# Kernel tuning notes

Measured on AMD Instinct MI355X. Metric: run time of the kernel, lower is better.

## Reference

```python
import jax, jax.numpy as jnp
import numpy as np

N_NODES = 50000
N_EDGES = 800000
F_IN = 128
HEADS = 4
C_OUT = 32
NEG_SLOPE = 0.2
BN_EPS = 1e-5


def _add_self_loops(edge_index, edge_attr, n):
    # PyG fill_value='mean': self-loop attr = mean of incoming edge attrs per node (0 if none)
    src, dst = edge_index[0], edge_index[1]
    deg = jax.ops.segment_sum(jnp.ones_like(edge_attr[:, 0]), dst, num_segments=n)
    loop_attr = jax.ops.segment_sum(edge_attr, dst, num_segments=n) / jnp.maximum(deg, 1.0)[:, None]
    loop = jnp.arange(n)
    src2 = jnp.concatenate([src, loop])
    dst2 = jnp.concatenate([dst, loop])
    attr2 = jnp.concatenate([edge_attr, loop_attr], axis=0)
    return src2, dst2, attr2


def _segment_softmax(logits, seg, n):
    m = jax.ops.segment_max(logits, seg, num_segments=n)
    m = jnp.where(jnp.isfinite(m), m, 0.0)
    ex = jnp.exp(logits - m[seg])
    s = jax.ops.segment_sum(ex, seg, num_segments=n)
    return ex / s[seg]


def _gatv2(x, src, dst, eattr, Wl, bl, Wr, br, We, att, bias, n):
    # x: [n, F]; returns [n, HEADS*C_OUT]
    xl = (x @ Wl + bl).reshape(n, HEADS, C_OUT)
    xr = (x @ Wr + br).reshape(n, HEADS, C_OUT)
    ea = (eattr @ We).reshape(-1, HEADS, C_OUT)
    xlj = xl[src]                                   # [E, H, C] gather
    msg = jax.nn.leaky_relu(xlj + xr[dst] + ea, NEG_SLOPE)
    logits = jnp.einsum('ehc,hc->eh', msg, att)     # [E, H]
    alpha = _segment_softmax(logits, dst, n)
    out = jax.ops.segment_sum(xlj * alpha[..., None], dst, num_segments=n)
    return out.reshape(n, HEADS * C_OUT) + bias


def _batchnorm(x, gamma, beta):
    mu = x.mean(axis=0)
    var = x.var(axis=0)
    return gamma * (x - mu) * jax.lax.rsqrt(var + BN_EPS) + beta


def setup_inputs() -> dict:
    key = jax.random.key(0)
    ks = jax.random.split(key, 20)
    HC = HEADS * C_OUT
    s = 0.05
    inp = {
        'emb': jax.random.normal(ks[0], (N_NODES, F_IN), dtype=jnp.float32),
        'edge_index': jax.random.randint(ks[1], (2, N_EDGES), 0, N_NODES, dtype=jnp.int64),
        'edge_weight': jax.random.uniform(ks[2], (N_EDGES, 1), dtype=jnp.float32),
        'Wl1': jax.random.normal(ks[3], (F_IN, HC)) * s,
        'bl1': jnp.zeros((HC,), jnp.float32),
        'Wr1': jax.random.normal(ks[4], (F_IN, HC)) * s,
        'br1': jnp.zeros((HC,), jnp.float32),
        'We1': jax.random.normal(ks[5], (1, HC)) * s,
        'att1': jax.random.normal(ks[6], (HEADS, C_OUT)) * s,
        'bias1': jnp.zeros((HC,), jnp.float32),
        'gamma1': jnp.ones((HC,), jnp.float32),
        'beta1': jnp.zeros((HC,), jnp.float32),
        'Wl2': jax.random.normal(ks[7], (HC, HC)) * s,
        'bl2': jnp.zeros((HC,), jnp.float32),
        'Wr2': jax.random.normal(ks[8], (HC, HC)) * s,
        'br2': jnp.zeros((HC,), jnp.float32),
        'We2': jax.random.normal(ks[9], (1, HC)) * s,
        'att2': jax.random.normal(ks[10], (HEADS, C_OUT)) * s,
        'bias2': jnp.zeros((HC,), jnp.float32),
    }
    return inp


def reference(emb, edge_index, edge_weight, Wl1, bl1, Wr1, br1, We1, att1, bias1,
              gamma1, beta1, Wl2, bl2, Wr2, br2, We2, att2, bias2):
    n = emb.shape[0]
    src, dst, eattr = _add_self_loops(edge_index, edge_weight, n)
    h1 = _gatv2(emb, src, dst, eattr, Wl1, bl1, Wr1, br1, We1, att1, bias1, n)
    h1 = jax.nn.elu(_batchnorm(h1, gamma1, beta1))
    h2 = _gatv2(h1, src, dst, eattr, Wl2, bl2, Wr2, br2, We2, att2, bias2, n)
    # fusion: mean over [input_emb, h1, h2] along stacked axis
    return (emb + h1 + h2) / 3.0
```

## Files before the change

kernel.cpp:

```cpp
#include <hip/hip_runtime.h>
#include <hip/hip_bf16.h>
#include <math.h>

#define N_NODES 50000
#define N_EDGES 800000
#define HC 128
#define SLOT 64

#define BM 128
#define NBX ((N_NODES + BM - 1) / BM)
#define NB_EDGE ((N_EDGES / 4 + 255) / 256)

typedef short bh8 __attribute__((ext_vector_type(8)));
typedef float f4 __attribute__((ext_vector_type(4)));
typedef float f2 __attribute__((ext_vector_type(2)));

__device__ __forceinline__ unsigned int pk2(float a, float b) {
  return (unsigned int)__bfloat16_as_ushort(__float2bfloat16(a)) |
         ((unsigned int)__bfloat16_as_ushort(__float2bfloat16(b)) << 16);
}

__global__ __launch_bounds__(256) void k_wprep(
    const float* __restrict__ Wl1, const float* __restrict__ Wr1,
    const float* __restrict__ Wl2, const float* __restrict__ Wr2,
    unsigned short* __restrict__ WtAll, int* __restrict__ cursor,
    float* __restrict__ chsum, float* __restrict__ chsq) {
  int gid = blockIdx.x * 256 + threadIdx.x;
  int m = gid >> 14;
  int idx = gid & 16383;
  const float* src = (m == 0) ? Wl1 : (m == 1) ? Wr1 : (m == 2) ? Wl2 : Wr2;
  int k = idx >> 7, n = idx & 127;
  WtAll[((size_t)m * HC + n) * HC + k] =
      __bfloat16_as_ushort(__float2bfloat16(src[k * HC + n]));
  if (gid < N_NODES) cursor[gid] = 0;
  if (gid < HC) { chsum[gid] = 0.f; chsq[gid] = 0.f; }
}

template <int LAYER2, int F8>
__device__ __forceinline__ void gemm_tile(
    int bx, const float* __restrict__ X, const unsigned short* __restrict__ Wt,
    const float* __restrict__ b0, const float* __restrict__ b1,
    void* __restrict__ Y0, float* __restrict__ Y1,
    const float* __restrict__ chsum, const float* __restrict__ chsq,
    const float* __restrict__ gamma, const float* __restrict__ beta) {
  __shared__ __align__(16) unsigned short Xls[128 * 128];
  __shared__ float ssc[HC], ssh[HC];
  int tid = threadIdx.x;
  if (LAYER2) {
    if (tid < HC) {
      float mu = chsum[tid] * (1.f / N_NODES);
      float var = chsq[tid] * (1.f / N_NODES) - mu * mu;
      float sc = gamma[tid] * rsqrtf(var + 1e-5f);
      ssc[tid] = sc;
      ssh[tid] = beta[tid] - mu * sc;
    }
    __syncthreads();
  }
  int row0 = bx * BM;
  {
    int r = tid >> 1;
    int ks = (tid & 1) * 64;
    int gr = row0 + r;
    const float* xp = X + (size_t)gr * HC + ks;
    int sw = r & 15;
#pragma unroll
    for (int i = 0; i < 4; ++i) {
      float f[16];
      if (gr < N_NODES) {
        *(float4*)&f[0] = *(const float4*)(xp + i * 16);
        *(float4*)&f[4] = *(const float4*)(xp + i * 16 + 4);
        *(float4*)&f[8] = *(const float4*)(xp + i * 16 + 8);
        *(float4*)&f[12] = *(const float4*)(xp + i * 16 + 12);
      } else {
#pragma unroll
        for (int j = 0; j < 16; ++j) f[j] = 0.f;
      }
      if (LAYER2) {
#pragma unroll
        for (int j = 0; j < 16; ++j) {
          float y = fmaf(f[j], ssc[ks + i * 16 + j], ssh[ks + i * 16 + j]);
          f[j] = (y > 0.f) ? y : (__expf(y) - 1.f);
        }
      }
      int kg = (ks >> 3) + i * 2;
      *(uint4*)&Xls[r * 128 + ((kg ^ sw) * 8)] =
          make_uint4(pk2(f[0], f[1]), pk2(f[2], f[3]), pk2(f[4], f[5]), pk2(f[6], f[7]));
      *(uint4*)&Xls[r * 128 + (((kg + 1) ^ sw) * 8)] =
          make_uint4(pk2(f[8], f[9]), pk2(f[10], f[11]), pk2(f[12], f[13]), pk2(f[14], f[15]));
    }
  }
  __syncthreads();
  int lane = tid & 63;
  int wv = tid >> 6;
  int lrow = lane & 15;
  int lq = lane >> 4;
  int rbase = wv * 32;
  bh8 afr[4][2];
#pragma unroll
  for (int kk = 0; kk < 4; ++kk) {
    int kg = kk * 4 + lq;
    afr[kk][0] = *(const bh8*)&Xls[(rbase + lrow) * 128 + ((kg ^ lrow) * 8)];
    afr[kk][1] = *(const bh8*)&Xls[(rbase + 16 + lrow) * 128 + ((kg ^ lrow) * 8)];
  }
#pragma unroll
  for (int half = 0; half < 2; ++half) {
    const unsigned short* wbase = Wt + half * (HC * HC);
    f4 acc[2][8];
#pragma unroll
    for (int mt = 0; mt < 2; ++mt)
#pragma unroll
      for (int nt = 0; nt < 8; ++nt) acc[mt][nt] = (f4){0.f, 0.f, 0.f, 0.f};
#pragma unroll
    for (int kk = 0; kk < 4; ++kk) {
      int kg = kk * 4 + lq;
      bh8 a0 = afr[kk][0];
      bh8 a1 = afr[kk][1];
#pragma unroll
      for (int nt = 0; nt < 8; ++nt) {
        bh8 b = *(const bh8*)(wbase + (nt * 16 + lrow) * HC + kg * 8);
        acc[0][nt] = __builtin_amdgcn_mfma_f32_16x16x32_bf16(a0, b, acc[0][nt], 0, 0, 0);
        acc[1][nt] = __builtin_amdgcn_mfma_f32_16x16x32_bf16(a1, b, acc[1][nt], 0, 0, 0);
      }
    }
    const float* bb = half ? b1 : b0;
    float bv[8];
#pragma unroll
    for (int nt = 0; nt < 8; ++nt) bv[nt] = bb[nt * 16 + lrow];
#pragma unroll
    for (int mt = 0; mt < 2; ++mt) {
#pragma unroll
      for (int rr = 0; rr < 4; ++rr) {
        int gr = row0 + rbase + mt * 16 + lq * 4 + rr;
        if (gr < N_NODES) {
          if (half == 0) {
            if (F8) {
#pragma unroll
              for (int nt = 0; nt < 8; ++nt) {
                float v = acc[mt][nt][rr] + bv[nt];
                int p = __builtin_amdgcn_cvt_pk_fp8_f32(v, v, 0, false);
                ((unsigned char*)Y0)[(size_t)gr * HC + nt * 16 + lrow] =
                    (unsigned char)(p & 0xff);
              }
            } else {
#pragma unroll
              for (int nt = 0; nt < 8; ++nt)
                ((unsigned short*)Y0)[(size_t)gr * HC + nt * 16 + lrow] =
                    __bfloat16_as_ushort(__float2bfloat16(acc[mt][nt][rr] + bv[nt]));
            }
          } else {
#pragma unroll
            for (int nt = 0; nt < 8; ++nt)
              Y1[(size_t)gr * HC + nt * 16 + lrow] = acc[mt][nt][rr] + bv[nt];
          }
        }
      }
    }
  }
}

__global__ __launch_bounds__(256) void k_g1prep(
    const float* __restrict__ X, const unsigned short* __restrict__ Wt,
    const float* __restrict__ b0, const float* __restrict__ b1,
    unsigned short* __restrict__ Y0b, float* __restrict__ Y1,
    const int* __restrict__ ei, const float* __restrict__ ew,
    int* __restrict__ cursor, unsigned int* __restrict__ slots) {
  int bid = blockIdx.x;
  if (bid < NBX) {
    gemm_tile<0, 0>(bid, X, Wt, b0, b1, (void*)Y0b, Y1, nullptr, nullptr,
                    nullptr, nullptr);
    return;
  }
  int e = ((bid - NBX) * 256 + threadIdx.x) * 4;
  if (e >= N_EDGES) return;
  int4 s4 = *(const int4*)(ei + e);
  int4 d4 = *(const int4*)(ei + N_EDGES + e);
  float4 w4 = *(const float4*)(ew + e);
  int ss[4] = {s4.x, s4.y, s4.z, s4.w};
  int dd[4] = {d4.x, d4.y, d4.z, d4.w};
  float ww[4] = {w4.x, w4.y, w4.z, w4.w};
  int pos[4];
#pragma unroll
  for (int i = 0; i < 4; ++i) pos[i] = atomicAdd(cursor + dd[i], 1);
#pragma unroll
  for (int i = 0; i < 4; ++i) {
    unsigned int wq = min((unsigned int)(ww[i] * 65536.f + 0.5f), 65535u);
    if (pos[i] < SLOT) {
      slots[(size_t)dd[i] * SLOT + pos[i]] = ((unsigned int)ss[i] << 16) | wq;
    }
  }
}

__global__ __launch_bounds__(256) void k_gemm2(
    const float* __restrict__ X, const unsigned short* __restrict__ Wt,
    const float* __restrict__ b0, const float* __restrict__ b1,
    unsigned char* __restrict__ Y0f8, float* __restrict__ Y1,
    const float* __restrict__ chsum, const float* __restrict__ chsq,
    const float* __restrict__ gamma, const float* __restrict__ beta) {
  gemm_tile<1, 1>(blockIdx.x, X, Wt, b0, b1, (void*)Y0f8, Y1, chsum, chsq,
                  gamma, beta);
}

template <int FINAL, int F8>
__global__ __launch_bounds__(256) void k_gat(
    const void* __restrict__ xlv, const float* __restrict__ xr,
    const int* __restrict__ cursor, const unsigned int* __restrict__ slots,
    const float* __restrict__ We, const float* __restrict__ att,
    const float* __restrict__ bias, float* __restrict__ out,
    const float* __restrict__ emb, const float* __restrict__ h1p,
    const float* __restrict__ chsum, const float* __restrict__ chsq,
    const float* __restrict__ gamma, const float* __restrict__ beta) {
  int g = threadIdx.x >> 5;
  int lane = threadIdx.x & 31;
  int n = blockIdx.x * 8 + g;
  int fi = n * 32 + lane;
  const uint2* xl2 = (const uint2*)xlv;
  const unsigned int* xf = (const unsigned int*)xlv;
  float4 xr4 = ((const float4*)xr)[fi];
  float4 we4 = ((const float4*)We)[lane];
  float4 at4 = ((const float4*)att)[lane];
  int deg = min(cursor[n], SLOT);
  int base = n * SLOT;
  int deg32 = min(deg, 32);

  unsigned int ev = (lane < deg32) ? slots[base + lane] : 0u;
  float evw = (float)(ev & 0xffffu) * (1.f / 65536.f);
  float wsum = evw;
#pragma unroll
  for (int m = 16; m >= 1; m >>= 1) wsum += __shfl_xor(wsum, m);

  float l = 0.f;
  float4 o = make_float4(0.f, 0.f, 0.f, 0.f);

  auto decode = [&](uint2 gc) -> float4 {
    float4 xlj;
    if (F8) {
      f2 ab = __builtin_amdgcn_cvt_pk_f32_fp8((int)gc.x, false);
      f2 cd = __builtin_amdgcn_cvt_pk_f32_fp8((int)gc.x, true);
      xlj.x = ab[0]; xlj.y = ab[1]; xlj.z = cd[0]; xlj.w = cd[1];
    } else {
      xlj.x = __uint_as_float(gc.x << 16);
      xlj.y = __uint_as_float(gc.x & 0xffff0000u);
      xlj.z = __uint_as_float(gc.y << 16);
      xlj.w = __uint_as_float(gc.y & 0xffff0000u);
    }
    return xlj;
  };
  auto edge_body = [&](float w, uint2 gc, bool valid) {
    float4 xlj = decode(gc);
    float4 v;
    v.x = fmaf(w, we4.x, xlj.x + xr4.x);
    v.y = fmaf(w, we4.y, xlj.y + xr4.y);
    v.z = fmaf(w, we4.z, xlj.z + xr4.z);
    v.w = fmaf(w, we4.w, xlj.w + xr4.w);
    v.x = fmaxf(v.x, 0.2f * v.x);
    v.y = fmaxf(v.y, 0.2f * v.y);
    v.z = fmaxf(v.z, 0.2f * v.z);
    v.w = fmaxf(v.w, 0.2f * v.w);
    float p = v.x * at4.x + v.y * at4.y + v.z * at4.z + v.w * at4.w;
    p += __shfl_xor(p, 1);
    p += __shfl_xor(p, 2);
    p += __shfl_xor(p, 4);
    float e = valid ? __expf(p) : 0.f;
    l += e;
    o.x = fmaf(e, xlj.x, o.x);
    o.y = fmaf(e, xlj.y, o.y);
    o.z = fmaf(e, xlj.z, o.z);
    o.w = fmaf(e, xlj.w, o.w);
  };
  auto fetch = [&](int j, uint2& qq, float& ww) {
    int jc = min(j, deg32 - 1);
    unsigned int evj = __shfl(ev, jc, 32);
    ww = (float)(evj & 0xffffu) * (1.f / 65536.f);
    int s = (int)(evj >> 16);
    if (F8) qq.x = xf[s * 32 + lane];
    else qq = xl2[s * 32 + lane];
  };

  if (deg32 > 0) {
    uint2 q0, q1, q2, q3;
    float w0, w1, w2, w3;
    fetch(0, q0, w0);
    fetch(1, q1, w1);
    fetch(2, q2, w2);
    fetch(3, q3, w3);
    for (int b = 0; b < deg32; b += 4) {
      uint2 c0 = q0, c1 = q1, c2 = q2, c3 = q3;
      float x0 = w0, x1 = w1, x2 = w2, x3 = w3;
      fetch(b + 4, q0, w0);
      fetch(b + 5, q1, w1);
      fetch(b + 6, q2, w2);
      fetch(b + 7, q3, w3);
      edge_body(x0, c0, true);
      edge_body(x1, c1, b + 1 < deg32);
      edge_body(x2, c2, b + 2 < deg32);
      edge_body(x3, c3, b + 3 < deg32);
    }
  }
  if (deg > 32) {
    for (int j = base + 32; j < base + deg; ++j) {
      unsigned int evj = slots[j];
      float w = (float)(evj & 0xffffu) * (1.f / 65536.f);
      wsum += w;
      int s = (int)(evj >> 16);
      uint2 gc;
      if (F8) gc.x = xf[s * 32 + lane];
      else gc = xl2[s * 32 + lane];
      edge_body(w, gc, true);
    }
  }
  {
    float wself = (deg > 0) ? wsum / (float)deg : 0.f;
    uint2 gs;
    if (F8) gs.x = xf[n * 32 + lane];
    else gs = xl2[n * 32 + lane];
    edge_body(wself, gs, true);
  }

  float inv = 1.f / l;
  float4 b4 = ((const float4*)bias)[lane];
  float4 r;
  r.x = fmaf(o.x, inv, b4.x);
  r.y = fmaf(o.y, inv, b4.y);
  r.z = fmaf(o.z, inv, b4.z);
  r.w = fmaf(o.w, inv, b4.w);
  if (FINAL) {
    float4 e4 = ((const float4*)emb)[fi];
    float4 h4 = ((const float4*)h1p)[fi];
    float4 cs = ((const float4*)chsum)[lane];
    float4 cq = ((const float4*)chsq)[lane];
    float4 gm = ((const float4*)gamma)[lane];
    float4 bt = ((const float4*)beta)[lane];
    const float invN = 1.f / N_NODES;
    float4 sc4, sh4;
    {
      float mu = cs.x * invN, var = cq.x * invN - mu * mu;
      sc4.x = gm.x * rsqrtf(var + 1e-5f); sh4.x = bt.x - mu * sc4.x;
      mu = cs.y * invN; var = cq.y * invN - mu * mu;
      sc4.y = gm.y * rsqrtf(var + 1e-5f); sh4.y = bt.y - mu * sc4.y;
      mu = cs.z * invN; var = cq.z * invN - mu * mu;
      sc4.z = gm.z * rsqrtf(var + 1e-5f); sh4.z = bt.z - mu * sc4.z;
      mu = cs.w * invN; var = cq.w * invN - mu * mu;
      sc4.w = gm.w * rsqrtf(var + 1e-5f); sh4.w = bt.w - mu * sc4.w;
    }
    float4 h;
    h.x = fmaf(h4.x, sc4.x, sh4.x);
    h.y = fmaf(h4.y, sc4.y, sh4.y);
    h.z = fmaf(h4.z, sc4.z, sh4.z);
    h.w = fmaf(h4.w, sc4.w, sh4.w);
    h.x = (h.x > 0.f) ? h.x : (__expf(h.x) - 1.f);
    h.y = (h.y > 0.f) ? h.y : (__expf(h.y) - 1.f);
    h.z = (h.z > 0.f) ? h.z : (__expf(h.z) - 1.f);
    h.w = (h.w > 0.f) ? h.w : (__expf(h.w) - 1.f);
    const float k3 = 1.f / 3.f;
    r.x = (e4.x + h.x + r.x) * k3;
    r.y = (e4.y + h.y + r.y) * k3;
    r.z = (e4.z + h.z + r.z) * k3;
    r.w = (e4.w + h.w + r.w) * k3;
  }
  ((float4*)out)[fi] = r;
}

#define BN_ROWS 200
__global__ __launch_bounds__(256) void k_bnstats(const float* __restrict__ h1,
                                                 float* __restrict__ chsum,
                                                 float* __restrict__ chsq) {
  int c = threadIdx.x & 127;
  int g = threadIdx.x >> 7;
  int r0 = blockIdx.x * BN_ROWS;
  float s = 0.f, q = 0.f;
  for (int r = r0 + g; r < r0 + BN_ROWS; r += 2) {
    float v = h1[(size_t)r * HC + c];
    s += v;
    q += v * v;
  }
  __shared__ float sh[256], shq[256];
  sh[threadIdx.x] = s;
  shq[threadIdx.x] = q;
  __syncthreads();
  if (g == 0) {
    atomicAdd(chsum + c, s + sh[threadIdx.x + 128]);
    atomicAdd(chsq + c, q + shq[threadIdx.x + 128]);
  }
}

extern "C" void kernel_launch(void* const* d_in, const int* in_sizes, int n_in,
                              void* d_out, int out_size, void* d_ws, size_t ws_size,
                              hipStream_t stream) {
  const float* emb = (const float*)d_in[0];
  const int* ei = (const int*)d_in[1];
  const float* ew = (const float*)d_in[2];
  const float* Wl1 = (const float*)d_in[3];
  const float* bl1 = (const float*)d_in[4];
  const float* Wr1 = (const float*)d_in[5];
  const float* br1 = (const float*)d_in[6];
  const float* We1 = (const float*)d_in[7];
  const float* att1 = (const float*)d_in[8];
  const float* bias1 = (const float*)d_in[9];
  const float* gamma1 = (const float*)d_in[10];
  const float* beta1 = (const float*)d_in[11];
  const float* Wl2 = (const float*)d_in[12];
  const float* bl2 = (const float*)d_in[13];
  const float* Wr2 = (const float*)d_in[14];
  const float* br2 = (const float*)d_in[15];
  const float* We2 = (const float*)d_in[16];
  const float* att2 = (const float*)d_in[17];
  const float* bias2 = (const float*)d_in[18];
  float* out = (float*)d_out;

  char* wsb = (char*)d_ws;
  size_t off = 0;
  auto alloc = [&](size_t bytes) -> void* {
    void* p = (void*)(wsb + off);
    off += (bytes + 255) & ~(size_t)255;
    return p;
  };
  int* cursor = (int*)alloc((size_t)N_NODES * 4);
  float* chsum = (float*)alloc(HC * 4);
  float* chsq = (float*)alloc(HC * 4);
  unsigned short* WtAll = (unsigned short*)alloc((size_t)4 * HC * HC * 2);
  unsigned int* slots = (unsigned int*)alloc((size_t)N_NODES * SLOT * 4);
  unsigned short* xlb = (unsigned short*)alloc((size_t)N_NODES * HC * 2);
  unsigned char* xlf8 = (unsigned char*)alloc((size_t)N_NODES * HC);
  float* xr = (float*)alloc((size_t)N_NODES * HC * 4);
  float* h1 = (float*)alloc((size_t)N_NODES * HC * 4);

  k_wprep<<<256, 256, 0, stream>>>(Wl1, Wr1, Wl2, Wr2, WtAll, cursor, chsum, chsq);
  k_g1prep<<<NBX + NB_EDGE, 256, 0, stream>>>(emb, WtAll, bl1, br1, xlb, xr,
                                              ei, ew, cursor, slots);
  k_gat<0, 0><<<N_NODES / 8, 256, 0, stream>>>(xlb, xr, cursor, slots, We1, att1,
                                               bias1, h1, nullptr, nullptr,
                                               nullptr, nullptr, nullptr, nullptr);
  k_bnstats<<<N_NODES / BN_ROWS, 256, 0, stream>>>(h1, chsum, chsq);
  k_gemm2<<<NBX, 256, 0, stream>>>(h1, WtAll + 2 * HC * HC, bl2, br2, xlf8, xr,
                                   chsum, chsq, gamma1, beta1);
  k_gat<1, 1><<<N_NODES / 8, 256, 0, stream>>>(xlf8, xr, cursor, slots, We2, att2,
                                               bias2, out, emb, h1, chsum, chsq,
                                               gamma1, beta1);
}
```

Measured before the change: 303.1 us.

## Store h1 in bf16, pad atomic cursors, stage W2 in LDS for gemm2

Layer-1 GAT output h1 is now written as bf16 instead of fp32. It is read back as bf16 by the BN stats kernel, the layer-2 GEMM and the final fusion, which halves that intermediate traffic. Per-node edge cursors are spread out with a stride of 16 ints to reduce atomic contention on shared cache lines, at the cost of a larger cursor buffer to zero. gemm2 becomes a standalone kernel that stages the weight tile in LDS with swizzling. The trade-off is extra precision loss in h1 (used in BN statistics and the final output) and more LDS per block in gemm2.

```diff
diff --git a/kernel.cpp b/kernel.cpp
--- a/kernel.cpp
+++ b/kernel.cpp
@@ -6,6 +6,7 @@
 #define N_EDGES 800000
 #define HC 128
 #define SLOT 64
+#define CSTRIDE 16
 
 #define BM 128
 #define NBX ((N_NODES + BM - 1) / BM)
@@ -19,6 +20,8 @@
   return (unsigned int)__bfloat16_as_ushort(__float2bfloat16(a)) |
          ((unsigned int)__bfloat16_as_ushort(__float2bfloat16(b)) << 16);
 }
+__device__ __forceinline__ float blo(unsigned int u) { return __uint_as_float(u << 16); }
+__device__ __forceinline__ float bhi(unsigned int u) { return __uint_as_float(u & 0xffff0000u); }
 
 __global__ __launch_bounds__(256) void k_wprep(
     const float* __restrict__ Wl1, const float* __restrict__ Wr1,
@@ -32,31 +35,41 @@
   int k = idx >> 7, n = idx & 127;
   WtAll[((size_t)m * HC + n) * HC + k] =
       __bfloat16_as_ushort(__float2bfloat16(src[k * HC + n]));
-  if (gid < N_NODES) cursor[gid] = 0;
+  for (int i = gid; i < N_NODES * CSTRIDE; i += 65536) cursor[i] = 0;
   if (gid < HC) { chsum[gid] = 0.f; chsq[gid] = 0.f; }
 }
 
-template <int LAYER2, int F8>
-__device__ __forceinline__ void gemm_tile(
-    int bx, const float* __restrict__ X, const unsigned short* __restrict__ Wt,
+__global__ __launch_bounds__(256) void k_g1prep(
+    const float* __restrict__ X, const unsigned short* __restrict__ Wt,
     const float* __restrict__ b0, const float* __restrict__ b1,
-    void* __restrict__ Y0, float* __restrict__ Y1,
-    const float* __restrict__ chsum, const float* __restrict__ chsq,
-    const float* __restrict__ gamma, const float* __restrict__ beta) {
+    unsigned short* __restrict__ Y0b, float* __restrict__ Y1,
+    const int* __restrict__ ei, const float* __restrict__ ew,
+    int* __restrict__ cursor, unsigned int* __restrict__ slots) {
+  int bid = blockIdx.x;
+  int tid = threadIdx.x;
+  if (bid >= NBX) {
+    int e = ((bid - NBX) * 256 + tid) * 4;
+    if (e >= N_EDGES) return;
+    int4 s4 = *(const int4*)(ei + e);
+    int4 d4 = *(const int4*)(ei + N_EDGES + e);
+    float4 w4 = *(const float4*)(ew + e);
+    int ss[4] = {s4.x, s4.y, s4.z, s4.w};
+    int dd[4] = {d4.x, d4.y, d4.z, d4.w};
+    float ww[4] = {w4.x, w4.y, w4.z, w4.w};
+    int pos[4];
+#pragma unroll
+    for (int i = 0; i < 4; ++i) pos[i] = atomicAdd(cursor + dd[i] * CSTRIDE, 1);
+#pragma unroll
+    for (int i = 0; i < 4; ++i) {
+      unsigned int wq = min((unsigned int)(ww[i] * 65536.f + 0.5f), 65535u);
+      if (pos[i] < SLOT) {
+        slots[(size_t)dd[i] * SLOT + pos[i]] = ((unsigned int)ss[i] << 16) | wq;
+      }
+    }
+    return;
+  }
   __shared__ __align__(16) unsigned short Xls[128 * 128];
-  __shared__ float ssc[HC], ssh[HC];
-  int tid = threadIdx.x;
-  if (LAYER2) {
-    if (tid < HC) {
-      float mu = chsum[tid] * (1.f / N_NODES);
-      float var = chsq[tid] * (1.f / N_NODES) - mu * mu;
-      float sc = gamma[tid] * rsqrtf(var + 1e-5f);
-      ssc[tid] = sc;
-      ssh[tid] = beta[tid] - mu * sc;
-    }
-    __syncthreads();
-  }
-  int row0 = bx * BM;
+  int row0 = bid * BM;
   {
     int r = tid >> 1;
     int ks = (tid & 1) * 64;
@@ -75,13 +88,6 @@
 #pragma unroll
         for (int j = 0; j < 16; ++j) f[j] = 0.f;
       }
-      if (LAYER2) {
-#pragma unroll
-        for (int j = 0; j < 16; ++j) {
-          float y = fmaf(f[j], ssc[ks + i * 16 + j], ssh[ks + i * 16 + j]);
-          f[j] = (y > 0.f) ? y : (__expf(y) - 1.f);
-        }
-      }
       int kg = (ks >> 3) + i * 2;
       *(uint4*)&Xls[r * 128 + ((kg ^ sw) * 8)] =
           make_uint4(pk2(f[0], f[1]), pk2(f[2], f[3]), pk2(f[4], f[5]), pk2(f[6], f[7]));
@@ -113,13 +119,11 @@
 #pragma unroll
     for (int kk = 0; kk < 4; ++kk) {
       int kg = kk * 4 + lq;
-      bh8 a0 = afr[kk][0];
-      bh8 a1 = afr[kk][1];
 #pragma unroll
       for (int nt = 0; nt < 8; ++nt) {
         bh8 b = *(const bh8*)(wbase + (nt * 16 + lrow) * HC + kg * 8);
-        acc[0][nt] = __builtin_amdgcn_mfma_f32_16x16x32_bf16(a0, b, acc[0][nt], 0, 0, 0);
-        acc[1][nt] = __builtin_amdgcn_mfma_f32_16x16x32_bf16(a1, b, acc[1][nt], 0, 0, 0);
+        acc[0][nt] = __builtin_amdgcn_mfma_f32_16x16x32_bf16(afr[kk][0], b, acc[0][nt], 0, 0, 0);
+        acc[1][nt] = __builtin_amdgcn_mfma_f32_16x16x32_bf16(afr[kk][1], b, acc[1][nt], 0, 0, 0);
       }
     }
     const float* bb = half ? b1 : b0;
@@ -133,20 +137,10 @@
         int gr = row0 + rbase + mt * 16 + lq * 4 + rr;
         if (gr < N_NODES) {
           if (half == 0) {
-            if (F8) {
-#pragma unroll
-              for (int nt = 0; nt < 8; ++nt) {
-                float v = acc[mt][nt][rr] + bv[nt];
-                int p = __builtin_amdgcn_cvt_pk_fp8_f32(v, v, 0, false);
-                ((unsigned char*)Y0)[(size_t)gr * HC + nt * 16 + lrow] =
-                    (unsigned char)(p & 0xff);
-              }
-            } else {
-#pragma unroll
-              for (int nt = 0; nt < 8; ++nt)
-                ((unsigned short*)Y0)[(size_t)gr * HC + nt * 16 + lrow] =
-                    __bfloat16_as_ushort(__float2bfloat16(acc[mt][nt][rr] + bv[nt]));
-            }
+#pragma unroll
+            for (int nt = 0; nt < 8; ++nt)
+              Y0b[(size_t)gr * HC + nt * 16 + lrow] =
+                  __bfloat16_as_ushort(__float2bfloat16(acc[mt][nt][rr] + bv[nt]));
           } else {
 #pragma unroll
             for (int nt = 0; nt < 8; ++nt)
@@ -158,46 +152,121 @@
   }
 }
 
-__global__ __launch_bounds__(256) void k_g1prep(
-    const float* __restrict__ X, const unsigned short* __restrict__ Wt,
-    const float* __restrict__ b0, const float* __restrict__ b1,
-    unsigned short* __restrict__ Y0b, float* __restrict__ Y1,
-    const int* __restrict__ ei, const float* __restrict__ ew,
-    int* __restrict__ cursor, unsigned int* __restrict__ slots) {
-  int bid = blockIdx.x;
-  if (bid < NBX) {
-    gemm_tile<0, 0>(bid, X, Wt, b0, b1, (void*)Y0b, Y1, nullptr, nullptr,
-                    nullptr, nullptr);
-    return;
-  }
-  int e = ((bid - NBX) * 256 + threadIdx.x) * 4;
-  if (e >= N_EDGES) return;
-  int4 s4 = *(const int4*)(ei + e);
-  int4 d4 = *(const int4*)(ei + N_EDGES + e);
-  float4 w4 = *(const float4*)(ew + e);
-  int ss[4] = {s4.x, s4.y, s4.z, s4.w};
-  int dd[4] = {d4.x, d4.y, d4.z, d4.w};
-  float ww[4] = {w4.x, w4.y, w4.z, w4.w};
-  int pos[4];
-#pragma unroll
-  for (int i = 0; i < 4; ++i) pos[i] = atomicAdd(cursor + dd[i], 1);
-#pragma unroll
-  for (int i = 0; i < 4; ++i) {
-    unsigned int wq = min((unsigned int)(ww[i] * 65536.f + 0.5f), 65535u);
-    if (pos[i] < SLOT) {
-      slots[(size_t)dd[i] * SLOT + pos[i]] = ((unsigned int)ss[i] << 16) | wq;
-    }
-  }
-}
-
 __global__ __launch_bounds__(256) void k_gemm2(
-    const float* __restrict__ X, const unsigned short* __restrict__ Wt,
+    const unsigned short* __restrict__ Xb, const unsigned short* __restrict__ Wt,
     const float* __restrict__ b0, const float* __restrict__ b1,
     unsigned char* __restrict__ Y0f8, float* __restrict__ Y1,
     const float* __restrict__ chsum, const float* __restrict__ chsq,
     const float* __restrict__ gamma, const float* __restrict__ beta) {
-  gemm_tile<1, 1>(blockIdx.x, X, Wt, b0, b1, (void*)Y0f8, Y1, chsum, chsq,
-                  gamma, beta);
+  __shared__ __align__(16) unsigned short Xls[128 * 128];
+  __shared__ __align__(16) unsigned short Wls[128 * 128];
+  __shared__ float ssc[HC], ssh[HC];
+  int tid = threadIdx.x;
+  if (tid < HC) {
+    float mu = chsum[tid] * (1.f / N_NODES);
+    float var = chsq[tid] * (1.f / N_NODES) - mu * mu;
+    float sc = gamma[tid] * rsqrtf(var + 1e-5f);
+    ssc[tid] = sc;
+    ssh[tid] = beta[tid] - mu * sc;
+  }
+  __syncthreads();
+  int row0 = blockIdx.x * BM;
+  {
+    int r = tid >> 1;
+    int ks = (tid & 1) * 64;
+    int gr = row0 + r;
+    const unsigned short* xp = Xb + (size_t)gr * HC + ks;
+    int sw = r & 15;
+#pragma unroll
+    for (int i = 0; i < 4; ++i) {
+      float f[16];
+      if (gr < N_NODES) {
+        uint4 ua = *(const uint4*)(xp + i * 16);
+        uint4 ub = *(const uint4*)(xp + i * 16 + 8);
+        f[0] = blo(ua.x); f[1] = bhi(ua.x); f[2] = blo(ua.y); f[3] = bhi(ua.y);
+        f[4] = blo(ua.z); f[5] = bhi(ua.z); f[6] = blo(ua.w); f[7] = bhi(ua.w);
+        f[8] = blo(ub.x); f[9] = bhi(ub.x); f[10] = blo(ub.y); f[11] = bhi(ub.y);
+        f[12] = blo(ub.z); f[13] = bhi(ub.z); f[14] = blo(ub.w); f[15] = bhi(ub.w);
+      } else {
+#pragma unroll
+        for (int j = 0; j < 16; ++j) f[j] = 0.f;
+      }
+#pragma unroll
+      for (int j = 0; j < 16; ++j) {
+        float y = fmaf(f[j], ssc[ks + i * 16 + j], ssh[ks + i * 16 + j]);
+        f[j] = (y > 0.f) ? y : (__expf(y) - 1.f);
+      }
+      int kg = (ks >> 3) + i * 2;
+      *(uint4*)&Xls[r * 128 + ((kg ^ sw) * 8)] =
+          make_uint4(pk2(f[0], f[1]), pk2(f[2], f[3]), pk2(f[4], f[5]), pk2(f[6], f[7]));
+      *(uint4*)&Xls[r * 128 + (((kg + 1) ^ sw) * 8)] =
+          make_uint4(pk2(f[8], f[9]), pk2(f[10], f[11]), pk2(f[12], f[13]), pk2(f[14], f[15]));
+    }
+  }
+  int lane = tid & 63;
+  int wv = tid >> 6;
+  int lrow = lane & 15;
+  int lq = lane >> 4;
+  int rbase = wv * 32;
+#pragma unroll
+  for (int half = 0; half < 2; ++half) {
+    if (half) __syncthreads();
+    {
+      int n = tid >> 1;
+      int ks = (tid & 1) * 64;
+      const unsigned short* wp = Wt + half * (HC * HC) + n * HC + ks;
+      int swn = n & 15;
+#pragma unroll
+      for (int g = 0; g < 8; ++g) {
+        uint4 v = *(const uint4*)(wp + g * 8);
+        int kg = (ks >> 3) + g;
+        *(uint4*)&Wls[n * 128 + ((kg ^ swn) * 8)] = v;
+      }
+    }
+    __syncthreads();
+    f4 acc[2][8];
+#pragma unroll
+    for (int mt = 0; mt < 2; ++mt)
+#pragma unroll
+      for (int nt = 0; nt < 8; ++nt) acc[mt][nt] = (f4){0.f, 0.f, 0.f, 0.f};
+#pragma unroll
+    for (int kk = 0; kk < 4; ++kk) {
+      int kg = kk * 4 + lq;
+      bh8 a0 = *(const bh8*)&Xls[(rbase + lrow) * 128 + ((kg ^ lrow) * 8)];
+      bh8 a1 = *(const bh8*)&Xls[(rbase + 16 + lrow) * 128 + ((kg ^ lrow) * 8)];
+#pragma unroll
+      for (int nt = 0; nt < 8; ++nt) {
+        bh8 b = *(const bh8*)&Wls[(nt * 16 + lrow) * 128 + ((kg ^ lrow) * 8)];
+        acc[0][nt] = __builtin_amdgcn_mfma_f32_16x16x32_bf16(a0, b, acc[0][nt], 0, 0, 0);
+        acc[1][nt] = __builtin_amdgcn_mfma_f32_16x16x32_bf16(a1, b, acc[1][nt], 0, 0, 0);
+      }
+    }
+    const float* bb = half ? b1 : b0;
+    float bv[8];
+#pragma unroll
+    for (int nt = 0; nt < 8; ++nt) bv[nt] = bb[nt * 16 + lrow];
+#pragma unroll
+    for (int mt = 0; mt < 2; ++mt) {
+#pragma unroll
+      for (int rr = 0; rr < 4; ++rr) {
+        int gr = row0 + rbase + mt * 16 + lq * 4 + rr;
+        if (gr < N_NODES) {
+          if (half == 0) {
+#pragma unroll
+            for (int nt = 0; nt < 8; ++nt) {
+              float v = acc[mt][nt][rr] + bv[nt];
+              int p = __builtin_amdgcn_cvt_pk_fp8_f32(v, v, 0, false);
+              Y0f8[(size_t)gr * HC + nt * 16 + lrow] = (unsigned char)(p & 0xff);
+            }
+          } else {
+#pragma unroll
+            for (int nt = 0; nt < 8; ++nt)
+              Y1[(size_t)gr * HC + nt * 16 + lrow] = acc[mt][nt][rr] + bv[nt];
+          }
+        }
+      }
+    }
+  }
 }
 
 template <int FINAL, int F8>
@@ -205,8 +274,8 @@
     const void* __restrict__ xlv, const float* __restrict__ xr,
     const int* __restrict__ cursor, const unsigned int* __restrict__ slots,
     const float* __restrict__ We, const float* __restrict__ att,
-    const float* __restrict__ bias, float* __restrict__ out,
-    const float* __restrict__ emb, const float* __restrict__ h1p,
+    const float* __restrict__ bias, void* __restrict__ out,
+    const float* __restrict__ emb, const unsigned short* __restrict__ h1p,
     const float* __restrict__ chsum, const float* __restrict__ chsq,
     const float* __restrict__ gamma, const float* __restrict__ beta) {
   int g = threadIdx.x >> 5;
@@ -218,7 +287,7 @@
   float4 xr4 = ((const float4*)xr)[fi];
   float4 we4 = ((const float4*)We)[lane];
   float4 at4 = ((const float4*)att)[lane];
-  int deg = min(cursor[n], SLOT);
+  int deg = min(cursor[n * CSTRIDE], SLOT);
   int base = n * SLOT;
   int deg32 = min(deg, 32);
 
@@ -238,10 +307,8 @@
       f2 cd = __builtin_amdgcn_cvt_pk_f32_fp8((int)gc.x, true);
       xlj.x = ab[0]; xlj.y = ab[1]; xlj.z = cd[0]; xlj.w = cd[1];
     } else {
-      xlj.x = __uint_as_float(gc.x << 16);
-      xlj.y = __uint_as_float(gc.x & 0xffff0000u);
-      xlj.z = __uint_as_float(gc.y << 16);
-      xlj.w = __uint_as_float(gc.y & 0xffff0000u);
+      xlj.x = blo(gc.x); xlj.y = bhi(gc.x);
+      xlj.z = blo(gc.y); xlj.w = bhi(gc.y);
     }
     return xlj;
   };
@@ -325,7 +392,9 @@
   r.w = fmaf(o.w, inv, b4.w);
   if (FINAL) {
     float4 e4 = ((const float4*)emb)[fi];
-    float4 h4 = ((const float4*)h1p)[fi];
+    uint2 hh = ((const uint2*)h1p)[fi];
+    float4 h4;
+    h4.x = blo(hh.x); h4.y = bhi(hh.x); h4.z = blo(hh.y); h4.w = bhi(hh.y);
     float4 cs = ((const float4*)chsum)[lane];
     float4 cq = ((const float4*)chsq)[lane];
     float4 gm = ((const float4*)gamma)[lane];
@@ -356,30 +425,42 @@
     r.y = (e4.y + h.y + r.y) * k3;
     r.z = (e4.z + h.z + r.z) * k3;
     r.w = (e4.w + h.w + r.w) * k3;
-  }
-  ((float4*)out)[fi] = r;
+    ((float4*)out)[fi] = r;
+  } else {
+    ((uint2*)out)[fi] = make_uint2(pk2(r.x, r.y), pk2(r.z, r.w));
+  }
 }
 
 #define BN_ROWS 200
-__global__ __launch_bounds__(256) void k_bnstats(const float* __restrict__ h1,
+__global__ __launch_bounds__(256) void k_bnstats(const unsigned short* __restrict__ h1b,
                                                  float* __restrict__ chsum,
                                                  float* __restrict__ chsq) {
-  int c = threadIdx.x & 127;
-  int g = threadIdx.x >> 7;
+  int c2 = threadIdx.x & 63;
+  int g = threadIdx.x >> 6;
   int r0 = blockIdx.x * BN_ROWS;
-  float s = 0.f, q = 0.f;
-  for (int r = r0 + g; r < r0 + BN_ROWS; r += 2) {
-    float v = h1[(size_t)r * HC + c];
-    s += v;
-    q += v * v;
-  }
-  __shared__ float sh[256], shq[256];
-  sh[threadIdx.x] = s;
-  shq[threadIdx.x] = q;
+  float s0 = 0.f, s1 = 0.f, q0 = 0.f, q1 = 0.f;
+  const unsigned int* h32 = (const unsigned int*)h1b;
+  for (int r = r0 + g; r < r0 + BN_ROWS; r += 4) {
+    unsigned int u = h32[(size_t)r * 64 + c2];
+    float a = blo(u), b = bhi(u);
+    s0 += a; q0 += a * a;
+    s1 += b; q1 += b * b;
+  }
+  __shared__ float sh[256][4];
+  sh[threadIdx.x][0] = s0; sh[threadIdx.x][1] = q0;
+  sh[threadIdx.x][2] = s1; sh[threadIdx.x][3] = q1;
   __syncthreads();
   if (g == 0) {
-    atomicAdd(chsum + c, s + sh[threadIdx.x + 128]);
-    atomicAdd(chsq + c, q + shq[threadIdx.x + 128]);
+    float ts0 = 0.f, tq0 = 0.f, ts1 = 0.f, tq1 = 0.f;
+#pragma unroll
+    for (int gg = 0; gg < 4; ++gg) {
+      ts0 += sh[gg * 64 + c2][0]; tq0 += sh[gg * 64 + c2][1];
+      ts1 += sh[gg * 64 + c2][2]; tq1 += sh[gg * 64 + c2][3];
+    }
+    atomicAdd(chsum + 2 * c2, ts0);
+    atomicAdd(chsq + 2 * c2, tq0);
+    atomicAdd(chsum + 2 * c2 + 1, ts1);
+    atomicAdd(chsq + 2 * c2 + 1, tq1);
   }
 }
 
@@ -414,7 +495,7 @@
     off += (bytes + 255) & ~(size_t)255;
     return p;
   };
-  int* cursor = (int*)alloc((size_t)N_NODES * 4);
+  int* cursor = (int*)alloc((size_t)N_NODES * CSTRIDE * 4);
   float* chsum = (float*)alloc(HC * 4);
   float* chsq = (float*)alloc(HC * 4);
   unsigned short* WtAll = (unsigned short*)alloc((size_t)4 * HC * HC * 2);
@@ -422,18 +503,18 @@
   unsigned short* xlb = (unsigned short*)alloc((size_t)N_NODES * HC * 2);
   unsigned char* xlf8 = (unsigned char*)alloc((size_t)N_NODES * HC);
   float* xr = (float*)alloc((size_t)N_NODES * HC * 4);
-  float* h1 = (float*)alloc((size_t)N_NODES * HC * 4);
+  unsigned short* h1b = (unsigned short*)alloc((size_t)N_NODES * HC * 2);
 
   k_wprep<<<256, 256, 0, stream>>>(Wl1, Wr1, Wl2, Wr2, WtAll, cursor, chsum, chsq);
   k_g1prep<<<NBX + NB_EDGE, 256, 0, stream>>>(emb, WtAll, bl1, br1, xlb, xr,
                                               ei, ew, cursor, slots);
   k_gat<0, 0><<<N_NODES / 8, 256, 0, stream>>>(xlb, xr, cursor, slots, We1, att1,
-                                               bias1, h1, nullptr, nullptr,
+                                               bias1, (void*)h1b, nullptr, nullptr,
                                                nullptr, nullptr, nullptr, nullptr);
-  k_bnstats<<<N_NODES / BN_ROWS, 256, 0, stream>>>(h1, chsum, chsq);
-  k_gemm2<<<NBX, 256, 0, stream>>>(h1, WtAll + 2 * HC * HC, bl2, br2, xlf8, xr,
+  k_bnstats<<<N_NODES / BN_ROWS, 256, 0, stream>>>(h1b, chsum, chsq);
+  k_gemm2<<<NBX, 256, 0, stream>>>(h1b, WtAll + 2 * HC * HC, bl2, br2, xlf8, xr,
                                    chsum, chsq, gamma1, beta1);
   k_gat<1, 1><<<N_NODES / 8, 256, 0, stream>>>(xlf8, xr, cursor, slots, We2, att2,
-                                               bias2, out, emb, h1, chsum, chsq,
-                                               gamma1, beta1);
-}
+                                               bias2, (void*)out, emb, h1b,
+                                               chsum, chsq, gamma1, beta1);
+}
```

After: 289.0 us. -4.7%, faster.
